# Performance work log

Measured on AMD Instinct MI355X. Metric: run time of the kernel, lower is better.

## Reference

```python
import jax, jax.numpy as jnp
import numpy as np

C, B, N, IN, OUT = 32, 32, 4096, 16, 32
NUM_ITERS = 3


def _squash(t, axis=-1):
    # scale = |t|^2 / (1 + |t|^2); out = scale * t / |t|
    sn = jnp.sum(t * t, axis=axis, keepdims=True)
    return (sn / (1.0 + sn)) * t / jnp.sqrt(sn)


def setup_inputs() -> dict:
    key = jax.random.key(0)
    k1, k2 = jax.random.split(key)
    x = jax.random.normal(k1, (B, N, IN), dtype=jnp.float32)
    route_weights = jax.random.normal(k2, (C, N, IN, OUT), dtype=jnp.float32)
    return {"x": x, "route_weights": route_weights}


def reference(x, route_weights):
    # priors[c,b,n,d] = sum_i x[b,n,i] * W[c,n,i,d]  (torch: [C,B,N,1,D], singleton dropped)
    priors = jnp.einsum('bni,cnio->cbno', x, route_weights)  # [C,B,N,D]
    # torch logits are [C,B,N,1,D] but constant over D (delta broadcasts), and the
    # custom softmax normalizes over dim=2 (route nodes N), so [C,B,N] is equivalent.
    logits = jnp.zeros(priors.shape[:3], dtype=priors.dtype)  # [C,B,N]
    outputs = None
    for i in range(NUM_ITERS):
        probs = jax.nn.softmax(logits, axis=2)  # softmax over route nodes (dim=2)
        s = jnp.sum(probs[..., None] * priors, axis=2, keepdims=True)  # [C,B,1,D]
        outputs = _squash(s, axis=-1)
        if i != NUM_ITERS - 1:
            logits = logits + jnp.sum(priors * outputs, axis=-1)  # agreement [C,B,N]
    return outputs[:, :, :, None, :]  # [C,B,1,1,D] to match torch output shape
```

## Files before the change

kernel.cpp:

```cpp
#include <hip/hip_runtime.h>
#include <math.h>


typedef _Float16 f16x8 __attribute__((ext_vector_type(8)));
typedef float f32x16 __attribute__((ext_vector_type(16)));

namespace {
constexpr int kC = 32, kB = 32, kN = 4096, kI = 16, kD = 32;
constexpr int CHUNKS = 32;
constexpr int CHUNK_N = kN / CHUNKS;
constexpr int PS = kB * kD + kB;
constexpr int GRID = kC * CHUNKS;
constexpr size_t XT_ELEMS = (size_t)kN * kB * kI;
constexpr size_t WT_ELEMS = (size_t)kC * kN * kI * kD;
constexpr size_t P_FLOATS = (size_t)kC * CHUNKS * PS;
constexpr size_t CV_FLOATS = (size_t)kC * kB * kD;
constexpr size_t WS_BYTES_MID = XT_ELEMS * 2 + (P_FLOATS + CV_FLOATS) * 4;
constexpr size_t WS_BYTES_BIG =
    (XT_ELEMS + WT_ELEMS) * 2 + (P_FLOATS + CV_FLOATS) * 4;
}

__device__ __forceinline__ f32x16 zero16() {
  f32x16 z;
#pragma unroll
  for (int r = 0; r < 16; ++r) z[r] = 0.f;
  return z;
}

__global__ __launch_bounds__(256) void k_xt(const float* __restrict__ x,
                                            _Float16* __restrict__ xt) {
  const int t = blockIdx.x * 256 + threadIdx.x;
  const int r = t >> 1, half = t & 1;
  const int b = r >> 12, n = r & 4095;
  const float4* s4 =
      reinterpret_cast<const float4*>(x) + (size_t)r * 4 + half * 2;
  const float4 f0 = s4[0], f1 = s4[1];
  f16x8 o;
  o[0] = (_Float16)f0.x; o[1] = (_Float16)f0.y;
  o[2] = (_Float16)f0.z; o[3] = (_Float16)f0.w;
  o[4] = (_Float16)f1.x; o[5] = (_Float16)f1.y;
  o[6] = (_Float16)f1.z; o[7] = (_Float16)f1.w;
  *reinterpret_cast<f16x8*>(xt + ((size_t)n * kB + b) * kI + half * 8) = o;
}

template <int MODE, bool EMIT>
__global__ __launch_bounds__(256) void k_sweep(const float* __restrict__ W,
                                               const _Float16* __restrict__ xt,
                                               const float* __restrict__ cumVec,
                                               float* __restrict__ partials,
                                               _Float16* __restrict__ Wt) {
  __shared__ float red[4][32][33];
  __shared__ float lred[4][32];
  const int bid = blockIdx.x;
  const int c = bid & 31;
  const int chunk = bid >> 5;
  const int tid = threadIdx.x;
  const int w = tid >> 6, l = tid & 63;
  const int m = l & 31, h = l >> 5;
  const int n0 = chunk * CHUNK_N;
  constexpr int TILES = CHUNK_N / 4;

  const float* wp = W + ((size_t)c * kN + n0 + w) * 512 + (h * 8) * 32 + m;
  const _Float16* xp = xt + ((size_t)(n0 + w)) * 512 + m * 16 + h * 8;
  _Float16* wtp =
      EMIT ? (Wt + ((size_t)c * kN + n0 + w) * 512 + (size_t)l * 8) : nullptr;

  float cvr[16];
  if (MODE) {
    const float* cvp = cumVec + (size_t)c * 1024 + m * 32;
#pragma unroll
    for (int r = 0; r < 16; ++r) cvr[r] = cvp[(r & 3) + 8 * (r >> 2) + 4 * h];
  }

  f32x16 accA = zero16(), accB = zero16();
  float lacc = 0.f;
  const f32x16 z = zero16();

  float rA0[8], rA1[8];
  f16x8 B0, B1;
#pragma unroll
  for (int j = 0; j < 8; ++j)
    rA0[j] = EMIT ? __builtin_nontemporal_load(wp + j * 32) : wp[j * 32];
  B0 = *reinterpret_cast<const f16x8*>(xp);
#pragma unroll
  for (int j = 0; j < 8; ++j)
    rA1[j] = EMIT ? __builtin_nontemporal_load(wp + 2048 + j * 32)
                  : wp[2048 + j * 32];
  B1 = *reinterpret_cast<const f16x8*>(xp + 2048);

#pragma unroll 1
  for (int t = 0; t < TILES; t += 2) {
    {
      f16x8 a;
#pragma unroll
      for (int j = 0; j < 8; ++j) a[j] = (_Float16)rA0[j];
      const f16x8 b = B0;
      const int tn = (t + 2 < TILES) ? t + 2 : 0;
#pragma unroll
      for (int j = 0; j < 8; ++j)
        rA0[j] = EMIT ? __builtin_nontemporal_load(wp + (size_t)tn * 2048 +
                                                   j * 32)
                      : wp[(size_t)tn * 2048 + j * 32];
      B0 = *reinterpret_cast<const f16x8*>(xp + (size_t)tn * 2048);
      if constexpr (EMIT)
        *reinterpret_cast<f16x8*>(wtp + (size_t)t * 2048) = a;
      if constexpr (MODE == 0) {
        accA = __builtin_amdgcn_mfma_f32_32x32x16_f16(a, b, accA, 0, 0, 0);
      } else {
        const f32x16 pr =
            __builtin_amdgcn_mfma_f32_32x32x16_f16(a, b, z, 0, 0, 0);
        float d0 = pr[0] * cvr[0], d1 = pr[1] * cvr[1];
        float d2 = pr[2] * cvr[2], d3 = pr[3] * cvr[3];
#pragma unroll
        for (int r = 4; r < 16; r += 4) {
          d0 = fmaf(pr[r + 0], cvr[r + 0], d0);
          d1 = fmaf(pr[r + 1], cvr[r + 1], d1);
          d2 = fmaf(pr[r + 2], cvr[r + 2], d2);
          d3 = fmaf(pr[r + 3], cvr[r + 3], d3);
        }
        float dp = (d0 + d1) + (d2 + d3);
        dp += __shfl_xor(dp, 32);
        const float e = __expf(dp);
        lacc += e;
#pragma unroll
        for (int r = 0; r < 16; ++r) accA[r] = fmaf(e, pr[r], accA[r]);
      }
    }
    {
      f16x8 a;
#pragma unroll
      for (int j = 0; j < 8; ++j) a[j] = (_Float16)rA1[j];
      const f16x8 b = B1;
      const int tn = (t + 3 < TILES) ? t + 3 : 0;
#pragma unroll
      for (int j = 0; j < 8; ++j)
        rA1[j] = EMIT ? __builtin_nontemporal_load(wp + (size_t)tn * 2048 +
                                                   j * 32)
                      : wp[(size_t)tn * 2048 + j * 32];
      B1 = *reinterpret_cast<const f16x8*>(xp + (size_t)tn * 2048);
      if constexpr (EMIT)
        *reinterpret_cast<f16x8*>(wtp + (size_t)(t + 1) * 2048) = a;
      if constexpr (MODE == 0) {
        accB = __builtin_amdgcn_mfma_f32_32x32x16_f16(a, b, accB, 0, 0, 0);
      } else {
        const f32x16 pr =
            __builtin_amdgcn_mfma_f32_32x32x16_f16(a, b, z, 0, 0, 0);
        float d0 = pr[0] * cvr[0], d1 = pr[1] * cvr[1];
        float d2 = pr[2] * cvr[2], d3 = pr[3] * cvr[3];
#pragma unroll
        for (int r = 4; r < 16; r += 4) {
          d0 = fmaf(pr[r + 0], cvr[r + 0], d0);
          d1 = fmaf(pr[r + 1], cvr[r + 1], d1);
          d2 = fmaf(pr[r + 2], cvr[r + 2], d2);
          d3 = fmaf(pr[r + 3], cvr[r + 3], d3);
        }
        float dp = (d0 + d1) + (d2 + d3);
        dp += __shfl_xor(dp, 32);
        const float e = __expf(dp);
        lacc += e;
#pragma unroll
        for (int r = 0; r < 16; ++r) accB[r] = fmaf(e, pr[r], accB[r]);
      }
    }
  }
#pragma unroll
  for (int r = 0; r < 16; ++r) accA[r] += accB[r];

#pragma unroll
  for (int r = 0; r < 16; ++r)
    red[w][(r & 3) + 8 * (r >> 2) + 4 * h][m] = accA[r];
  if (MODE && h == 0) lred[w][m] = lacc;
  __syncthreads();

  float* Pp = partials + ((size_t)c * CHUNKS + chunk) * PS;
#pragma unroll
  for (int e = tid; e < 1024; e += 256) {
    const int d = e >> 5, bb = e & 31;
    Pp[e] = red[0][d][bb] + red[1][d][bb] + red[2][d][bb] + red[3][d][bb];
  }
  if (MODE && tid < 32)
    Pp[1024 + tid] = lred[0][tid] + lred[1][tid] + lred[2][tid] + lred[3][tid];
}

__global__ __launch_bounds__(256) void k_sweep_wt(
    const _Float16* __restrict__ Wt, const _Float16* __restrict__ xt,
    const float* __restrict__ cumVec, float* __restrict__ partials) {
  __shared__ float red[4][32][33];
  __shared__ float lred[4][32];
  const int bid = blockIdx.x;
  const int c = bid & 31;
  const int chunk = bid >> 5;
  const int tid = threadIdx.x;
  const int w = tid >> 6, l = tid & 63;
  const int m = l & 31, h = l >> 5;
  const int n0 = chunk * CHUNK_N;
  constexpr int TILES = CHUNK_N / 4;

  const _Float16* wp = Wt + ((size_t)c * kN + n0 + w) * 512 + (size_t)l * 8;
  const _Float16* xp = xt + ((size_t)(n0 + w)) * 512 + m * 16 + h * 8;

  float cvr[16];
  const float* cvp = cumVec + (size_t)c * 1024 + m * 32;
#pragma unroll
  for (int r = 0; r < 16; ++r) cvr[r] = cvp[(r & 3) + 8 * (r >> 2) + 4 * h];

  f32x16 accA = zero16(), accB = zero16();
  float lacc = 0.f;
  const f32x16 z = zero16();

  f16x8 A0, A1, B0, B1;
  A0 = *reinterpret_cast<const f16x8*>(wp);
  B0 = *reinterpret_cast<const f16x8*>(xp);
  A1 = *reinterpret_cast<const f16x8*>(wp + 2048);
  B1 = *reinterpret_cast<const f16x8*>(xp + 2048);

#pragma unroll 1
  for (int t = 0; t < TILES; t += 2) {
    {
      const f16x8 a = A0;
      const f16x8 b = B0;
      const int tn = (t + 2 < TILES) ? t + 2 : 0;
      A0 = *reinterpret_cast<const f16x8*>(wp + (size_t)tn * 2048);
      B0 = *reinterpret_cast<const f16x8*>(xp + (size_t)tn * 2048);
      const f32x16 pr =
          __builtin_amdgcn_mfma_f32_32x32x16_f16(a, b, z, 0, 0, 0);
      float d0 = pr[0] * cvr[0], d1 = pr[1] * cvr[1];
      float d2 = pr[2] * cvr[2], d3 = pr[3] * cvr[3];
#pragma unroll
      for (int r = 4; r < 16; r += 4) {
        d0 = fmaf(pr[r + 0], cvr[r + 0], d0);
        d1 = fmaf(pr[r + 1], cvr[r + 1], d1);
        d2 = fmaf(pr[r + 2], cvr[r + 2], d2);
        d3 = fmaf(pr[r + 3], cvr[r + 3], d3);
      }
      float dp = (d0 + d1) + (d2 + d3);
      dp += __shfl_xor(dp, 32);
      const float e = __expf(dp);
      lacc += e;
#pragma unroll
      for (int r = 0; r < 16; ++r) accA[r] = fmaf(e, pr[r], accA[r]);
    }
    {
      const f16x8 a = A1;
      const f16x8 b = B1;
      const int tn = (t + 3 < TILES) ? t + 3 : 0;
      A1 = *reinterpret_cast<const f16x8*>(wp + (size_t)tn * 2048);
      B1 = *reinterpret_cast<const f16x8*>(xp + (size_t)tn * 2048);
      const f32x16 pr =
          __builtin_amdgcn_mfma_f32_32x32x16_f16(a, b, z, 0, 0, 0);
      float d0 = pr[0] * cvr[0], d1 = pr[1] * cvr[1];
      float d2 = pr[2] * cvr[2], d3 = pr[3] * cvr[3];
#pragma unroll
      for (int r = 4; r < 16; r += 4) {
        d0 = fmaf(pr[r + 0], cvr[r + 0], d0);
        d1 = fmaf(pr[r + 1], cvr[r + 1], d1);
        d2 = fmaf(pr[r + 2], cvr[r + 2], d2);
        d3 = fmaf(pr[r + 3], cvr[r + 3], d3);
      }
      float dp = (d0 + d1) + (d2 + d3);
      dp += __shfl_xor(dp, 32);
      const float e = __expf(dp);
      lacc += e;
#pragma unroll
      for (int r = 0; r < 16; ++r) accB[r] = fmaf(e, pr[r], accB[r]);
    }
  }
#pragma unroll
  for (int r = 0; r < 16; ++r) accA[r] += accB[r];

#pragma unroll
  for (int r = 0; r < 16; ++r)
    red[w][(r & 3) + 8 * (r >> 2) + 4 * h][m] = accA[r];
  if (h == 0) lred[w][m] = lacc;
  __syncthreads();

  float* Pp = partials + ((size_t)c * CHUNKS + chunk) * PS;
#pragma unroll
  for (int e = tid; e < 1024; e += 256) {
    const int d = e >> 5, bb = e & 31;
    Pp[e] = red[0][d][bb] + red[1][d][bb] + red[2][d][bb] + red[3][d][bb];
  }
  if (tid < 32)
    Pp[1024 + tid] = lred[0][tid] + lred[1][tid] + lred[2][tid] + lred[3][tid];
}

template <int K>
__global__ __launch_bounds__(1024) void k_reduce(
    const float* __restrict__ partials, float* __restrict__ CV,
    float* __restrict__ out) {
  const int c = blockIdx.x;
  const int t = threadIdx.x;
  const int b = t >> 5, d = t & 31;
  const float* Pc = partials + (size_t)c * CHUNKS * PS;
  float s = 0.f;
#pragma unroll 4
  for (int ch = 0; ch < CHUNKS; ++ch) s += Pc[(size_t)ch * PS + d * 32 + b];
  float inv;
  if constexpr (K == 0) {
    inv = 1.0f / (float)kN;
  } else {
    float lb = 0.f;
#pragma unroll 4
    for (int ch = 0; ch < CHUNKS; ++ch) lb += Pc[(size_t)ch * PS + 1024 + b];
    inv = 1.0f / lb;
  }
  const float sv = s * inv;
  float sn = sv * sv;
  sn += __shfl_xor(sn, 1);
  sn += __shfl_xor(sn, 2);
  sn += __shfl_xor(sn, 4);
  sn += __shfl_xor(sn, 8);
  sn += __shfl_xor(sn, 16);
  const float coef = sqrtf(sn) / (1.0f + sn);
  const float o = sv * coef;
  if constexpr (K == 2)
    out[(size_t)c * 1024 + t] = o;
  else if constexpr (K == 0)
    CV[(size_t)c * 1024 + t] = o;
  else
    CV[(size_t)c * 1024 + t] += o;
}

namespace v1 {
constexpr int BG = 4, NSLOT = 128, THREADS1 = NSLOT * 8;
template <int MODE>
__device__ __forceinline__ void sweep_pass(const float* __restrict__ Wc,
                                           const float* __restrict__ x, int b0,
                                           int tid, int nslot, int dg,
                                           float (*red)[8][20], float (*sS)[kD],
                                           float* sL, const float (*sVec)[kD]) {
  float acc[BG][4];
  float lv[BG];
#pragma unroll
  for (int b = 0; b < BG; ++b) {
    lv[b] = 0.f;
#pragma unroll
    for (int j = 0; j < 4; ++j) acc[b][j] = 0.f;
  }
  float vec[BG][4];
  if (MODE) {
#pragma unroll
    for (int b = 0; b < BG; ++b)
#pragma unroll
      for (int j = 0; j < 4; ++j) vec[b][j] = sVec[b][4 * dg + j];
  }
#pragma unroll 1
  for (int n = nslot; n < kN; n += NSLOT) {
    const float* Wn = Wc + (size_t)n * (kI * kD) + 4 * dg;
    float pr[BG][4];
#pragma unroll
    for (int b = 0; b < BG; ++b)
#pragma unroll
      for (int j = 0; j < 4; ++j) pr[b][j] = 0.f;
#pragma unroll
    for (int iq = 0; iq < 4; ++iq) {
      float4 wv[4];
#pragma unroll
      for (int r = 0; r < 4; ++r)
        wv[r] = *reinterpret_cast<const float4*>(Wn + (4 * iq + r) * kD);
#pragma unroll
      for (int b = 0; b < BG; ++b) {
        const float4 xv = *reinterpret_cast<const float4*>(
            x + ((size_t)(b0 + b) * kN + n) * kI + 4 * iq);
        const float xsv[4] = {xv.x, xv.y, xv.z, xv.w};
#pragma unroll
        for (int r = 0; r < 4; ++r) {
          pr[b][0] = fmaf(xsv[r], wv[r].x, pr[b][0]);
          pr[b][1] = fmaf(xsv[r], wv[r].y, pr[b][1]);
          pr[b][2] = fmaf(xsv[r], wv[r].z, pr[b][2]);
          pr[b][3] = fmaf(xsv[r], wv[r].w, pr[b][3]);
        }
      }
    }
    if (MODE == 0) {
#pragma unroll
      for (int b = 0; b < BG; ++b)
#pragma unroll
        for (int j = 0; j < 4; ++j) acc[b][j] += pr[b][j];
    } else {
#pragma unroll
      for (int b = 0; b < BG; ++b) {
        float dp = pr[b][0] * vec[b][0] + pr[b][1] * vec[b][1] +
                   pr[b][2] * vec[b][2] + pr[b][3] * vec[b][3];
        dp += __shfl_xor(dp, 1);
        dp += __shfl_xor(dp, 2);
        dp += __shfl_xor(dp, 4);
        const float e = __expf(dp);
        lv[b] += e;
        acc[b][0] = fmaf(e, pr[b][0], acc[b][0]);
        acc[b][1] = fmaf(e, pr[b][1], acc[b][1]);
        acc[b][2] = fmaf(e, pr[b][2], acc[b][2]);
        acc[b][3] = fmaf(e, pr[b][3], acc[b][3]);
      }
    }
  }
#pragma unroll
  for (int b = 0; b < BG; ++b) {
#pragma unroll
    for (int j = 0; j < 4; ++j) {
      float v = acc[b][j];
      v += __shfl_xor(v, 8);
      v += __shfl_xor(v, 16);
      v += __shfl_xor(v, 32);
      acc[b][j] = v;
    }
    if (MODE) {
      float v = lv[b];
      v += __shfl_xor(v, 8);
      v += __shfl_xor(v, 16);
      v += __shfl_xor(v, 32);
      lv[b] = v;
    }
  }
  const int lane = tid & 63;
  const int wv_id = tid >> 6;
  if ((lane >> 3) == 0) {
#pragma unroll
    for (int b = 0; b < BG; ++b) {
#pragma unroll
      for (int j = 0; j < 4; ++j) red[wv_id][dg][4 * b + j] = acc[b][j];
      if (MODE) red[wv_id][dg][16 + b] = lv[b];
    }
  }
  __syncthreads();
  if (tid < 128) {
    const int dgc = tid >> 4, e = tid & 15;
    float s = 0.f;
#pragma unroll
    for (int w = 0; w < 16; ++w) s += red[w][dgc][e];
    sS[e >> 2][4 * dgc + (e & 3)] = s;
  }
  if (MODE && tid >= 128 && tid < 128 + BG) {
    const int b = tid - 128;
    float s = 0.f;
#pragma unroll
    for (int w = 0; w < 16; ++w) s += red[w][0][16 + b];
    sL[b] = s;
  }
  __syncthreads();
}

__global__ __launch_bounds__(THREADS1, 4) void caps_route_kernel(
    const float* __restrict__ x, const float* __restrict__ W,
    float* __restrict__ out) {
  __shared__ float red[16][8][20];
  __shared__ float sS[BG][kD];
  __shared__ float sVec[BG][kD];
  __shared__ float sL[BG];
  const int i = blockIdx.x;
  const int xcd = i & 7;
  const int j = i >> 3;
  const int c = xcd + 8 * (j >> 3);
  const int b0 = 4 * (j & 7);
  const int tid = threadIdx.x;
  const int nslot = tid >> 3;
  const int dg = tid & 7;
  const float* Wc = W + (size_t)c * kN * kI * kD;
  sweep_pass<0>(Wc, x, b0, tid, nslot, dg, red, sS, sL, sVec);
  if (tid < BG) {
    const int b = tid;
    float sval[kD], sn = 0.f;
    const float inv = 1.0f / (float)kN;
#pragma unroll
    for (int d = 0; d < kD; ++d) {
      sval[d] = sS[b][d] * inv;
      sn += sval[d] * sval[d];
    }
    const float coef = sqrtf(sn) / (1.0f + sn);
#pragma unroll
    for (int d = 0; d < kD; ++d) sVec[b][d] = sval[d] * coef;
  }
  __syncthreads();
  sweep_pass<1>(Wc, x, b0, tid, nslot, dg, red, sS, sL, sVec);
  if (tid < BG) {
    const int b = tid;
    float sval[kD], sn = 0.f;
    const float inv = 1.0f / sL[b];
#pragma unroll
    for (int d = 0; d < kD; ++d) {
      sval[d] = sS[b][d] * inv;
      sn += sval[d] * sval[d];
    }
    const float coef = sqrtf(sn) / (1.0f + sn);
#pragma unroll
    for (int d = 0; d < kD; ++d) sVec[b][d] += sval[d] * coef;
  }
  __syncthreads();
  sweep_pass<1>(Wc, x, b0, tid, nslot, dg, red, sS, sL, sVec);
  if (tid < BG) {
    const int b = tid;
    float sval[kD], sn = 0.f;
    const float inv = 1.0f / sL[b];
#pragma unroll
    for (int d = 0; d < kD; ++d) {
      sval[d] = sS[b][d] * inv;
      sn += sval[d] * sval[d];
    }
    const float coef = sqrtf(sn) / (1.0f + sn);
    float* o = out + ((size_t)c * kB + (b0 + b)) * kD;
#pragma unroll
    for (int d = 0; d < kD; ++d) o[d] = sval[d] * coef;
  }
}
}

extern "C" void kernel_launch(void* const* d_in, const int* in_sizes, int n_in,
                              void* d_out, int out_size, void* d_ws,
                              size_t ws_size, hipStream_t stream) {
  const float* x = (const float*)d_in[0];
  const float* W = (const float*)d_in[1];
  float* out = (float*)d_out;
  (void)in_sizes; (void)n_in; (void)out_size;

  if (ws_size >= WS_BYTES_BIG) {
    _Float16* xt = (_Float16*)d_ws;
    _Float16* Wt = xt + XT_ELEMS;
    float* P = (float*)(Wt + WT_ELEMS);
    float* CV = P + P_FLOATS;

    k_xt<<<GRID, 256, 0, stream>>>(x, xt);
    k_sweep<0, true><<<GRID, 256, 0, stream>>>(W, xt, nullptr, P, Wt);
    k_reduce<0><<<kC, 1024, 0, stream>>>(P, CV, nullptr);
    k_sweep_wt<<<GRID, 256, 0, stream>>>(Wt, xt, CV, P);
    k_reduce<1><<<kC, 1024, 0, stream>>>(P, CV, nullptr);
    k_sweep_wt<<<GRID, 256, 0, stream>>>(Wt, xt, CV, P);
    k_reduce<2><<<kC, 1024, 0, stream>>>(P, nullptr, out);
    return;
  }

  if (ws_size >= WS_BYTES_MID) {
    _Float16* xt = (_Float16*)d_ws;
    float* P = (float*)(xt + XT_ELEMS);
    float* CV = P + P_FLOATS;

    k_xt<<<GRID, 256, 0, stream>>>(x, xt);
    k_sweep<0, false><<<GRID, 256, 0, stream>>>(W, xt, nullptr, P, nullptr);
    k_reduce<0><<<kC, 1024, 0, stream>>>(P, CV, nullptr);
    k_sweep<1, false><<<GRID, 256, 0, stream>>>(W, xt, CV, P, nullptr);
    k_reduce<1><<<kC, 1024, 0, stream>>>(P, CV, nullptr);
    k_sweep<1, false><<<GRID, 256, 0, stream>>>(W, xt, CV, P, nullptr);
    k_reduce<2><<<kC, 1024, 0, stream>>>(P, nullptr, out);
    return;
  }

  v1::caps_route_kernel<<<256, v1::THREADS1, 0, stream>>>(x, W, out);
}
```

Before: 201.0 us.

## Fuse sweep and reduce stages into one cooperative kernel with grid syncs

Replaces the six separate sweep/reduce launches with a single cooperative kernel that separates the stages with grid.sync. The goal is to remove kernel launch gaps and tail effects between the three routing iterations. The reduce step now runs on 32 blocks with 8 threads per (b), handling four d values each, while the other blocks idle at the barrier. Separate partial and cumulative-vector buffers are used per stage, and the kernel falls back to the old path if the grid cannot be co-resident. Grid-wide barriers add their own cost, and launch_bounds(256,4) may limit registers.

```diff
diff --git a/kernel.cpp b/kernel.cpp
--- a/kernel.cpp
+++ b/kernel.cpp
@@ -1,5 +1,8 @@
 #include <hip/hip_runtime.h>
+#include <hip/hip_cooperative_groups.h>
 #include <math.h>
+
+namespace cg = cooperative_groups;
 
 
 typedef _Float16 f16x8 __attribute__((ext_vector_type(8)));
@@ -18,6 +21,8 @@
 constexpr size_t WS_BYTES_MID = XT_ELEMS * 2 + (P_FLOATS + CV_FLOATS) * 4;
 constexpr size_t WS_BYTES_BIG =
     (XT_ELEMS + WT_ELEMS) * 2 + (P_FLOATS + CV_FLOATS) * 4;
+constexpr size_t WS_BYTES_COOP =
+    (XT_ELEMS + WT_ELEMS) * 2 + (3 * P_FLOATS + 2 * CV_FLOATS) * 4;
 }
 
 __device__ __forceinline__ f32x16 zero16() {
@@ -42,6 +47,263 @@
   o[6] = (_Float16)f1.z; o[7] = (_Float16)f1.w;
   *reinterpret_cast<f16x8*>(xt + ((size_t)n * kB + b) * kI + half * 8) = o;
 }
+
+
+__device__ __forceinline__ void mega_sweep0(const float* __restrict__ W,
+                                            const _Float16* __restrict__ xt,
+                                            _Float16* __restrict__ Wt,
+                                            float* __restrict__ P,
+                                            float (*red)[32][33], int c,
+                                            int chunk, int tid) {
+  const int w = tid >> 6, l = tid & 63;
+  const int m = l & 31, h = l >> 5;
+  const int n0 = chunk * CHUNK_N;
+  constexpr int TILES = CHUNK_N / 4;
+
+  const float* wp = W + ((size_t)c * kN + n0 + w) * 512 + (h * 8) * 32 + m;
+  const _Float16* xp = xt + ((size_t)(n0 + w)) * 512 + m * 16 + h * 8;
+  _Float16* wtp = Wt + ((size_t)c * kN + n0 + w) * 512 + (size_t)l * 8;
+
+  f32x16 accA = zero16(), accB = zero16();
+
+  float rA0[8], rA1[8];
+  f16x8 B0, B1;
+#pragma unroll
+  for (int j = 0; j < 8; ++j) rA0[j] = __builtin_nontemporal_load(wp + j * 32);
+  B0 = *reinterpret_cast<const f16x8*>(xp);
+#pragma unroll
+  for (int j = 0; j < 8; ++j)
+    rA1[j] = __builtin_nontemporal_load(wp + 2048 + j * 32);
+  B1 = *reinterpret_cast<const f16x8*>(xp + 2048);
+
+#pragma unroll 1
+  for (int t = 0; t < TILES; t += 2) {
+    {
+      f16x8 a;
+#pragma unroll
+      for (int j = 0; j < 8; ++j) a[j] = (_Float16)rA0[j];
+      const f16x8 b = B0;
+      const int tn = (t + 2 < TILES) ? t + 2 : 0;
+#pragma unroll
+      for (int j = 0; j < 8; ++j)
+        rA0[j] = __builtin_nontemporal_load(wp + (size_t)tn * 2048 + j * 32);
+      B0 = *reinterpret_cast<const f16x8*>(xp + (size_t)tn * 2048);
+      *reinterpret_cast<f16x8*>(wtp + (size_t)t * 2048) = a;
+      accA = __builtin_amdgcn_mfma_f32_32x32x16_f16(a, b, accA, 0, 0, 0);
+    }
+    {
+      f16x8 a;
+#pragma unroll
+      for (int j = 0; j < 8; ++j) a[j] = (_Float16)rA1[j];
+      const f16x8 b = B1;
+      const int tn = (t + 3 < TILES) ? t + 3 : 0;
+#pragma unroll
+      for (int j = 0; j < 8; ++j)
+        rA1[j] = __builtin_nontemporal_load(wp + (size_t)tn * 2048 + j * 32);
+      B1 = *reinterpret_cast<const f16x8*>(xp + (size_t)tn * 2048);
+      *reinterpret_cast<f16x8*>(wtp + (size_t)(t + 1) * 2048) = a;
+      accB = __builtin_amdgcn_mfma_f32_32x32x16_f16(a, b, accB, 0, 0, 0);
+    }
+  }
+#pragma unroll
+  for (int r = 0; r < 16; ++r) accA[r] += accB[r];
+
+#pragma unroll
+  for (int r = 0; r < 16; ++r)
+    red[w][(r & 3) + 8 * (r >> 2) + 4 * h][m] = accA[r];
+  __syncthreads();
+
+  float* Pp = P + ((size_t)c * CHUNKS + chunk) * PS;
+#pragma unroll
+  for (int e = tid; e < 1024; e += 256) {
+    const int d = e >> 5, bb = e & 31;
+    Pp[e] = red[0][d][bb] + red[1][d][bb] + red[2][d][bb] + red[3][d][bb];
+  }
+  __syncthreads();
+}
+
+__device__ __forceinline__ void mega_sweep_wt(
+    const _Float16* __restrict__ Wt, const _Float16* __restrict__ xt,
+    const float* __restrict__ cumVec, float* __restrict__ P,
+    float (*red)[32][33], float (*lred)[32], int c, int chunk, int tid) {
+  const int w = tid >> 6, l = tid & 63;
+  const int m = l & 31, h = l >> 5;
+  const int n0 = chunk * CHUNK_N;
+  constexpr int TILES = CHUNK_N / 4;
+
+  const _Float16* wp = Wt + ((size_t)c * kN + n0 + w) * 512 + (size_t)l * 8;
+  const _Float16* xp = xt + ((size_t)(n0 + w)) * 512 + m * 16 + h * 8;
+
+  float cvr[16];
+  const float* cvp = cumVec + (size_t)c * 1024 + m * 32;
+#pragma unroll
+  for (int r = 0; r < 16; ++r) cvr[r] = cvp[(r & 3) + 8 * (r >> 2) + 4 * h];
+
+  f32x16 accA = zero16(), accB = zero16();
+  float lacc = 0.f;
+  const f32x16 z = zero16();
+
+  f16x8 A0, A1, B0, B1;
+  A0 = *reinterpret_cast<const f16x8*>(wp);
+  B0 = *reinterpret_cast<const f16x8*>(xp);
+  A1 = *reinterpret_cast<const f16x8*>(wp + 2048);
+  B1 = *reinterpret_cast<const f16x8*>(xp + 2048);
+
+#pragma unroll 1
+  for (int t = 0; t < TILES; t += 2) {
+    {
+      const f16x8 a = A0;
+      const f16x8 b = B0;
+      const int tn = (t + 2 < TILES) ? t + 2 : 0;
+      A0 = *reinterpret_cast<const f16x8*>(wp + (size_t)tn * 2048);
+      B0 = *reinterpret_cast<const f16x8*>(xp + (size_t)tn * 2048);
+      const f32x16 pr =
+          __builtin_amdgcn_mfma_f32_32x32x16_f16(a, b, z, 0, 0, 0);
+      float d0 = pr[0] * cvr[0], d1 = pr[1] * cvr[1];
+      float d2 = pr[2] * cvr[2], d3 = pr[3] * cvr[3];
+#pragma unroll
+      for (int r = 4; r < 16; r += 4) {
+        d0 = fmaf(pr[r + 0], cvr[r + 0], d0);
+        d1 = fmaf(pr[r + 1], cvr[r + 1], d1);
+        d2 = fmaf(pr[r + 2], cvr[r + 2], d2);
+        d3 = fmaf(pr[r + 3], cvr[r + 3], d3);
+      }
+      float dp = (d0 + d1) + (d2 + d3);
+      dp += __shfl_xor(dp, 32);
+      const float e = __expf(dp);
+      lacc += e;
+#pragma unroll
+      for (int r = 0; r < 16; ++r) accA[r] = fmaf(e, pr[r], accA[r]);
+    }
+    {
+      const f16x8 a = A1;
+      const f16x8 b = B1;
+      const int tn = (t + 3 < TILES) ? t + 3 : 0;
+      A1 = *reinterpret_cast<const f16x8*>(wp + (size_t)tn * 2048);
+      B1 = *reinterpret_cast<const f16x8*>(xp + (size_t)tn * 2048);
+      const f32x16 pr =
+          __builtin_amdgcn_mfma_f32_32x32x16_f16(a, b, z, 0, 0, 0);
+      float d0 = pr[0] * cvr[0], d1 = pr[1] * cvr[1];
+      float d2 = pr[2] * cvr[2], d3 = pr[3] * cvr[3];
+#pragma unroll
+      for (int r = 4; r < 16; r += 4) {
+        d0 = fmaf(pr[r + 0], cvr[r + 0], d0);
+        d1 = fmaf(pr[r + 1], cvr[r + 1], d1);
+        d2 = fmaf(pr[r + 2], cvr[r + 2], d2);
+        d3 = fmaf(pr[r + 3], cvr[r + 3], d3);
+      }
+      float dp = (d0 + d1) + (d2 + d3);
+      dp += __shfl_xor(dp, 32);
+      const float e = __expf(dp);
+      lacc += e;
+#pragma unroll
+      for (int r = 0; r < 16; ++r) accB[r] = fmaf(e, pr[r], accB[r]);
+    }
+  }
+#pragma unroll
+  for (int r = 0; r < 16; ++r) accA[r] += accB[r];
+
+#pragma unroll
+  for (int r = 0; r < 16; ++r)
+    red[w][(r & 3) + 8 * (r >> 2) + 4 * h][m] = accA[r];
+  if (h == 0) lred[w][m] = lacc;
+  __syncthreads();
+
+  float* Pp = P + ((size_t)c * CHUNKS + chunk) * PS;
+#pragma unroll
+  for (int e = tid; e < 1024; e += 256) {
+    const int d = e >> 5, bb = e & 31;
+    Pp[e] = red[0][d][bb] + red[1][d][bb] + red[2][d][bb] + red[3][d][bb];
+  }
+  if (tid < 32)
+    Pp[1024 + tid] = lred[0][tid] + lred[1][tid] + lred[2][tid] + lred[3][tid];
+  __syncthreads();
+}
+
+template <int K>
+__device__ __forceinline__ void mega_reduce(const float* __restrict__ P,
+                                            float* __restrict__ CVout,
+                                            float* __restrict__ out,
+                                            float (&cvrun)[4], int c, int t) {
+  const int b = t >> 3, dg = t & 7;
+  const float* Pc = P + (size_t)c * CHUNKS * PS;
+  float s0 = 0.f, s1 = 0.f, s2 = 0.f, s3 = 0.f, lb = 0.f;
+#pragma unroll 4
+  for (int ch = 0; ch < CHUNKS; ++ch) {
+    const float* base = Pc + (size_t)ch * PS;
+    s0 += base[(dg + 0) * 32 + b];
+    s1 += base[(dg + 8) * 32 + b];
+    s2 += base[(dg + 16) * 32 + b];
+    s3 += base[(dg + 24) * 32 + b];
+    if (K != 0 && dg == 0) lb += base[1024 + b];
+  }
+  float inv;
+  if constexpr (K == 0) {
+    inv = 1.0f / (float)kN;
+  } else {
+    lb = __shfl(lb, (t & 63) & 56);
+    inv = 1.0f / lb;
+  }
+  const float v0 = s0 * inv, v1 = s1 * inv, v2 = s2 * inv, v3 = s3 * inv;
+  float sn = v0 * v0 + v1 * v1 + v2 * v2 + v3 * v3;
+  sn += __shfl_xor(sn, 1);
+  sn += __shfl_xor(sn, 2);
+  sn += __shfl_xor(sn, 4);
+  const float coef = sqrtf(sn) / (1.0f + sn);
+  const size_t o0 = (size_t)c * 1024 + b * 32 + dg;
+  if constexpr (K == 0) {
+    cvrun[0] = v0 * coef; cvrun[1] = v1 * coef;
+    cvrun[2] = v2 * coef; cvrun[3] = v3 * coef;
+    CVout[o0 + 0] = cvrun[0];  CVout[o0 + 8] = cvrun[1];
+    CVout[o0 + 16] = cvrun[2]; CVout[o0 + 24] = cvrun[3];
+  } else if constexpr (K == 1) {
+    cvrun[0] += v0 * coef; cvrun[1] += v1 * coef;
+    cvrun[2] += v2 * coef; cvrun[3] += v3 * coef;
+    CVout[o0 + 0] = cvrun[0];  CVout[o0 + 8] = cvrun[1];
+    CVout[o0 + 16] = cvrun[2]; CVout[o0 + 24] = cvrun[3];
+  } else {
+    out[o0 + 0] = v0 * coef;  out[o0 + 8] = v1 * coef;
+    out[o0 + 16] = v2 * coef; out[o0 + 24] = v3 * coef;
+  }
+}
+
+__global__ __launch_bounds__(256, 4) void k_mega(
+    const float* __restrict__ W, const _Float16* __restrict__ xt,
+    _Float16* __restrict__ Wt, float* __restrict__ P0, float* __restrict__ P1,
+    float* __restrict__ P2, float* __restrict__ CVa, float* __restrict__ CVb,
+    float* __restrict__ out) {
+  __shared__ float red[4][32][33];
+  __shared__ float lred[4][32];
+  cg::grid_group grid = cg::this_grid();
+  const int bid = blockIdx.x;
+  const int c = bid & 31;
+  const int chunk = bid >> 5;
+  const int tid = threadIdx.x;
+  float cvrun[4] = {0.f, 0.f, 0.f, 0.f};
+
+  mega_sweep0(W, xt, Wt, P0, red, c, chunk, tid);
+  __threadfence();
+  grid.sync();
+
+  if (bid < 32) mega_reduce<0>(P0, CVa, nullptr, cvrun, bid, tid);
+  __threadfence();
+  grid.sync();
+
+  mega_sweep_wt(Wt, xt, CVa, P1, red, lred, c, chunk, tid);
+  __threadfence();
+  grid.sync();
+
+  if (bid < 32) mega_reduce<1>(P1, CVb, nullptr, cvrun, bid, tid);
+  __threadfence();
+  grid.sync();
+
+  mega_sweep_wt(Wt, xt, CVb, P2, red, lred, c, chunk, tid);
+  __threadfence();
+  grid.sync();
+
+  if (bid < 32) mega_reduce<2>(P2, nullptr, out, cvrun, bid, tid);
+}
+
 
 template <int MODE, bool EMIT>
 __global__ __launch_bounds__(256) void k_sweep(const float* __restrict__ W,
@@ -191,97 +453,7 @@
   const int c = bid & 31;
   const int chunk = bid >> 5;
   const int tid = threadIdx.x;
-  const int w = tid >> 6, l = tid & 63;
-  const int m = l & 31, h = l >> 5;
-  const int n0 = chunk * CHUNK_N;
-  constexpr int TILES = CHUNK_N / 4;
-
-  const _Float16* wp = Wt + ((size_t)c * kN + n0 + w) * 512 + (size_t)l * 8;
-  const _Float16* xp = xt + ((size_t)(n0 + w)) * 512 + m * 16 + h * 8;
-
-  float cvr[16];
-  const float* cvp = cumVec + (size_t)c * 1024 + m * 32;
-#pragma unroll
-  for (int r = 0; r < 16; ++r) cvr[r] = cvp[(r & 3) + 8 * (r >> 2) + 4 * h];
-
-  f32x16 accA = zero16(), accB = zero16();
-  float lacc = 0.f;
-  const f32x16 z = zero16();
-
-  f16x8 A0, A1, B0, B1;
-  A0 = *reinterpret_cast<const f16x8*>(wp);
-  B0 = *reinterpret_cast<const f16x8*>(xp);
-  A1 = *reinterpret_cast<const f16x8*>(wp + 2048);
-  B1 = *reinterpret_cast<const f16x8*>(xp + 2048);
-
-#pragma unroll 1
-  for (int t = 0; t < TILES; t += 2) {
-    {
-      const f16x8 a = A0;
-      const f16x8 b = B0;
-      const int tn = (t + 2 < TILES) ? t + 2 : 0;
-      A0 = *reinterpret_cast<const f16x8*>(wp + (size_t)tn * 2048);
-      B0 = *reinterpret_cast<const f16x8*>(xp + (size_t)tn * 2048);
-      const f32x16 pr =
-          __builtin_amdgcn_mfma_f32_32x32x16_f16(a, b, z, 0, 0, 0);
-      float d0 = pr[0] * cvr[0], d1 = pr[1] * cvr[1];
-      float d2 = pr[2] * cvr[2], d3 = pr[3] * cvr[3];
-#pragma unroll
-      for (int r = 4; r < 16; r += 4) {
-        d0 = fmaf(pr[r + 0], cvr[r + 0], d0);
-        d1 = fmaf(pr[r + 1], cvr[r + 1], d1);
-        d2 = fmaf(pr[r + 2], cvr[r + 2], d2);
-        d3 = fmaf(pr[r + 3], cvr[r + 3], d3);
-      }
-      float dp = (d0 + d1) + (d2 + d3);
-      dp += __shfl_xor(dp, 32);
-      const float e = __expf(dp);
-      lacc += e;
-#pragma unroll
-      for (int r = 0; r < 16; ++r) accA[r] = fmaf(e, pr[r], accA[r]);
-    }
-    {
-      const f16x8 a = A1;
-      const f16x8 b = B1;
-      const int tn = (t + 3 < TILES) ? t + 3 : 0;
-      A1 = *reinterpret_cast<const f16x8*>(wp + (size_t)tn * 2048);
-      B1 = *reinterpret_cast<const f16x8*>(xp + (size_t)tn * 2048);
-      const f32x16 pr =
-          __builtin_amdgcn_mfma_f32_32x32x16_f16(a, b, z, 0, 0, 0);
-      float d0 = pr[0] * cvr[0], d1 = pr[1] * cvr[1];
-      float d2 = pr[2] * cvr[2], d3 = pr[3] * cvr[3];
-#pragma unroll
-      for (int r = 4; r < 16; r += 4) {
-        d0 = fmaf(pr[r + 0], cvr[r + 0], d0);
-        d1 = fmaf(pr[r + 1], cvr[r + 1], d1);
-        d2 = fmaf(pr[r + 2], cvr[r + 2], d2);
-        d3 = fmaf(pr[r + 3], cvr[r + 3], d3);
-      }
-      float dp = (d0 + d1) + (d2 + d3);
-      dp += __shfl_xor(dp, 32);
-      const float e = __expf(dp);
-      lacc += e;
-#pragma unroll
-      for (int r = 0; r < 16; ++r) accB[r] = fmaf(e, pr[r], accB[r]);
-    }
-  }
-#pragma unroll
-  for (int r = 0; r < 16; ++r) accA[r] += accB[r];
-
-#pragma unroll
-  for (int r = 0; r < 16; ++r)
-    red[w][(r & 3) + 8 * (r >> 2) + 4 * h][m] = accA[r];
-  if (h == 0) lred[w][m] = lacc;
-  __syncthreads();
-
-  float* Pp = partials + ((size_t)c * CHUNKS + chunk) * PS;
-#pragma unroll
-  for (int e = tid; e < 1024; e += 256) {
-    const int d = e >> 5, bb = e & 31;
-    Pp[e] = red[0][d][bb] + red[1][d][bb] + red[2][d][bb] + red[3][d][bb];
-  }
-  if (tid < 32)
-    Pp[1024 + tid] = lred[0][tid] + lred[1][tid] + lred[2][tid] + lred[3][tid];
+  mega_sweep_wt(Wt, xt, cumVec, partials, red, lred, c, chunk, tid);
 }
 
 template <int K>
@@ -512,6 +684,37 @@
   float* out = (float*)d_out;
   (void)in_sizes; (void)n_in; (void)out_size;
 
+  static int s_coop = -1;
+  if (s_coop < 0) {
+    int dev = 0;
+    (void)hipGetDevice(&dev);
+    int nCU = 0;
+    (void)hipDeviceGetAttribute(&nCU, hipDeviceAttributeMultiprocessorCount,
+                                dev);
+    int maxB = 0;
+    (void)hipOccupancyMaxActiveBlocksPerMultiprocessor(&maxB, k_mega, 256, 0);
+    s_coop = (nCU > 0 && maxB > 0 && (size_t)nCU * maxB >= (size_t)GRID) ? 1
+                                                                         : 0;
+  }
+
+  if (s_coop == 1 && ws_size >= WS_BYTES_COOP) {
+    _Float16* xt = (_Float16*)d_ws;
+    _Float16* Wt = xt + XT_ELEMS;
+    float* P0 = (float*)(Wt + WT_ELEMS);
+    float* P1 = P0 + P_FLOATS;
+    float* P2 = P1 + P_FLOATS;
+    float* CVa = P2 + P_FLOATS;
+    float* CVb = CVa + CV_FLOATS;
+
+    k_xt<<<GRID, 256, 0, stream>>>(x, xt);
+    void* args[] = {(void*)&W,  (void*)&xt,  (void*)&Wt,
+                    (void*)&P0, (void*)&P1,  (void*)&P2,
+                    (void*)&CVa, (void*)&CVb, (void*)&out};
+    if (hipLaunchCooperativeKernel(k_mega, dim3(GRID), dim3(256), args, 0,
+                                   stream) == hipSuccess)
+      return;
+  }
+
   if (ws_size >= WS_BYTES_BIG) {
     _Float16* xt = (_Float16*)d_ws;
     _Float16* Wt = xt + XT_ELEMS;
```

New measurement: 200.9 us. About the same (-0.0%).
